# Performance work log

Measured on AMD Instinct MI355X. Metric: run time of the kernel, lower is better.

Reference implementation:

```python
import jax, jax.numpy as jnp
import numpy as np

P_MIN = 0.8        # minimum cumulative probability mass kept per row
THRESHOLD = 1e-10  # drop matches with probability below this
EPS = 1e-6         # distance clamp (matches dist.clamp(min=1e-6) in backward)

B, N, M, D = 4, 4096, 4096, 3


def setup_inputs() -> dict:
    key = jax.random.key(0)
    kx, ky = jax.random.split(key)
    x = jax.random.normal(kx, (B, N, D), dtype=jnp.float32)
    y = jax.random.normal(ky, (B, M, D), dtype=jnp.float32)
    return {"x": x, "y": y}


def _pairwise_dist(x, y):
    # ||x_i - y_j|| via Gram trick; avoids materializing [B,N,M,D] diff tensor.
    sq = (
        jnp.sum(x * x, axis=-1)[:, :, None]
        + jnp.sum(y * y, axis=-1)[:, None, :]
        - 2.0 * jnp.einsum("bnd,bmd->bnm", x, y)
    )
    return jnp.sqrt(jnp.maximum(sq, EPS * EPS))  # [B, N, M]


def _sparse_match_weights(d):
    # Row-wise soft matching probabilities over targets j.
    p = jax.nn.softmax(-d, axis=-1)  # [B, N, M]
    # Keep the most-probable entries per row until cumulative mass reaches P_MIN
    # (the dense, jit-friendly equivalent of the COO compaction in the kernel).
    order = jnp.argsort(-p, axis=-1)
    p_sorted = jnp.take_along_axis(p, order, axis=-1)
    csum = jnp.cumsum(p_sorted, axis=-1)
    keep_sorted = (csum - p_sorted) < P_MIN  # include entry that crosses P_MIN
    inv = jnp.argsort(order, axis=-1)
    keep = jnp.take_along_axis(keep_sorted, inv, axis=-1)
    return jnp.where(keep & (p > THRESHOLD), p, 0.0)  # sparse COO values, dense layout


def reference(x, y):
    d = _pairwise_dist(x, y)                     # [B, N, M]
    w = jax.lax.stop_gradient(_sparse_match_weights(d))  # weights are constants in bwd
    loss = jnp.sum(w * d)                        # scalar matching loss
    return loss
```

## Files before the change

kernel.cpp:

```cpp
#include <hip/hip_runtime.h>


#define MCOLS 4096
#define KPT   64
#define WPB   4
#define P_MIN 0.8f

__device__ __forceinline__ float waveSum(float v) {
    #pragma unroll
    for (int o = 32; o > 0; o >>= 1) v += __shfl_xor(v, o, 64);
    return v;
}
__device__ __forceinline__ float waveMax(float v) {
    #pragma unroll
    for (int o = 32; o > 0; o >>= 1) v = fmaxf(v, __shfl_xor(v, o, 64));
    return v;
}

__global__ __launch_bounds__(WPB * 64) void apml_row_wave(
        const float* __restrict__ x, const float* __restrict__ y,
        float* __restrict__ out) {
    __shared__ __align__(16) float scomp[WPB * 64];
    __shared__ float wacc[WPB];

    const int tid  = threadIdx.x;
    const int wid  = tid >> 6;
    const int lane = tid & 63;
    const int row  = blockIdx.x * WPB + wid;
    const int b    = row >> 12;

    const float x0 = x[row * 3 + 0];
    const float x1 = x[row * 3 + 1];
    const float x2 = x[row * 3 + 2];
    const float* yb = y + (size_t)b * MCOLS * 3;

    float p[KPT];
    float zl = 0.0f, pml = 0.0f;
    #pragma unroll
    for (int k = 0; k < KPT; ++k) {
        const int j = k * 64 + lane;
        const float y0 = yb[j * 3 + 0];
        const float y1 = yb[j * 3 + 1];
        const float y2 = yb[j * 3 + 2];
        const float dx = x0 - y0, dy = x1 - y1, dz = x2 - y2;
        const float sq = fmaxf(dx * dx + dy * dy + dz * dz, 1e-12f);
        const float pk = __expf(-sqrtf(sq));
        p[k] = pk;
        zl  += pk;
        pml  = fmaxf(pml, pk);
    }
    const float Z    = waveSum(zl);
    const float pmax = waveMax(pml);
    const float target = P_MIN * Z;

    float sl = 0.0f, sh = __uint_as_float(__float_as_uint(pmax) + 1u);
    float Gl = Z,    Gh = 0.0f;
    int   Cl = MCOLS, Ch = 0;

    for (int it = 0; it < 16 && (Cl - Ch) > 64; ++it) {
        float s;
        if (it & 1) {
            s = 0.5f * (sl + sh);
        } else {
            const float den = fmaxf(Gl - Gh, 1e-30f);
            s = sl + (sh - sl) * ((Gl - target) / den);
        }
        if (!(s > sl && s < sh)) s = 0.5f * (sl + sh);
        if (!(s > sl && s < sh)) break;

        float m = 0.0f;
        int   c = 0;
        #pragma unroll
        for (int k = 0; k < KPT; ++k) {
            const bool ge = (p[k] >= s);
            m += ge ? p[k] : 0.0f;
            c += (int)__popcll(__ballot(ge));
        }
        m = waveSum(m);
        if (m >= target) { sl = s; Gl = m; Cl = c; }
        else             { sh = s; Gh = m; Ch = c; }
    }

    int C = 0;
    #pragma unroll
    for (int k = 0; k < KPT; ++k) {
        const bool band = (p[k] >= sl) && (p[k] < sh);
        const unsigned long long mk = __ballot(band);
        if (band) {
            const unsigned mlo = (unsigned)mk, mhi = (unsigned)(mk >> 32);
            const int within = __builtin_amdgcn_mbcnt_hi(
                                   mhi, __builtin_amdgcn_mbcnt_lo(mlo, 0));
            const int pos = C + within;
            if (pos < 64) scomp[wid * 64 + pos] = p[k];
        }
        C += (int)__popcll(mk);
    }
    __builtin_amdgcn_s_waitcnt(0);
    const bool valid = (lane < C) && (lane < 64);
    const float cp = valid ? scomp[wid * 64 + lane] : 0.0f;

    float pstar, mb = 0.0f;
    int   cnt = 1;
    bool  haveTie;

    if (C > 64) {
        pstar = (sl > 0.0f) ? __uint_as_float(__float_as_uint(sl) - 1u) : 0.0f;
        haveTie = false;
    } else {
        float lo_s = sl, hi_s = sh, lo_G = Gl, hi_G = Gh;
        int   lo_C = Cl, hi_C = Ch;
        for (int it = 0; it < 12 && (lo_C - hi_C) > 2; ++it) {
            float s;
            if (it & 1) {
                s = 0.5f * (lo_s + hi_s);
            } else {
                const float den = fmaxf(lo_G - hi_G, 1e-30f);
                s = lo_s + (hi_s - lo_s) * ((lo_G - target) / den);
            }
            if (!(s > lo_s && s < hi_s)) s = 0.5f * (lo_s + hi_s);
            if (!(s > lo_s && s < hi_s)) break;

            const bool ge = valid && (cp >= s);
            const int  c  = Ch + (int)__popcll(__ballot(ge));
            const float m = Gh + waveSum(ge ? cp : 0.0f);
            if (m >= target) { lo_s = s; lo_G = m; lo_C = c; }
            else             { hi_s = s; hi_G = m; hi_C = c; }
        }

        float scur = hi_s, M = hi_G;
        bool ok = false;
        pstar = lo_s;
        for (int e = 0; e < 80; ++e) {
            const float v = waveMax((valid && cp < scur) ? cp : 0.0f);
            if (!(v > 0.0f)) break;
            const int cv = (int)__popcll(__ballot(valid && (cp == v)));
            const float Mn = M + v * (float)cv;
            if (Mn >= target) { pstar = v; mb = M; cnt = cv; ok = true; break; }
            M = Mn; scur = v;
        }
        haveTie = ok;
        if (!ok) {
            pstar = (lo_s > 0.0f) ? __uint_as_float(__float_as_uint(lo_s) - 1u)
                                  : 0.0f;
        }
    }

    float spd = 0.0f;
    #pragma unroll
    for (int k = 0; k < KPT; ++k) {
        const float t = (p[k] > pstar) ? p[k] : 1.0f;
        spd += t * (-__logf(t));
    }
    spd = waveSum(spd);

    if (lane == 0) {
        float tie = 0.0f;
        if (haveTie) {
            const float R = (target - mb) / pstar;
            int q = (int)ceilf(R);
            if (q < 1) q = 1;
            if (q > cnt) q = cnt;
            tie = (float)q * pstar * (-__logf(pstar));
        }
        wacc[wid] = (spd + tie) / Z;
    }
    __syncthreads();
    if (tid == 0) {
        atomicAdd(out, wacc[0] + wacc[1] + wacc[2] + wacc[3]);
    }
}

extern "C" void kernel_launch(void* const* d_in, const int* in_sizes, int n_in,
                              void* d_out, int out_size, void* d_ws, size_t ws_size,
                              hipStream_t stream) {
    const float* x = (const float*)d_in[0];
    const float* y = (const float*)d_in[1];
    float* out = (float*)d_out;

    const int nrows = in_sizes[0] / 3;
    const int nblocks = nrows / WPB;

    hipMemsetAsync(out, 0, sizeof(float), stream);
    apml_row_wave<<<nblocks, WPB * 64, 0, stream>>>(x, y, out);
}
```

Measured before the change: 175.4 us.

## Use DPP reductions, sampled threshold pre-search, and wider 256-entry compaction band

```diff
diff --git a/kernel.cpp b/kernel.cpp
--- a/kernel.cpp
+++ b/kernel.cpp
@@ -6,21 +6,34 @@
 #define WPB   4
 #define P_MIN 0.8f
 
-__device__ __forceinline__ float waveSum(float v) {
-    #pragma unroll
-    for (int o = 32; o > 0; o >>= 1) v += __shfl_xor(v, o, 64);
-    return v;
-}
-__device__ __forceinline__ float waveMax(float v) {
-    #pragma unroll
-    for (int o = 32; o > 0; o >>= 1) v = fmaxf(v, __shfl_xor(v, o, 64));
-    return v;
+template <int CTRL, int RM, int BM, bool BC>
+__device__ __forceinline__ float dpp_mov0(float x) {
+    return __int_as_float(__builtin_amdgcn_update_dpp(
+        0, __float_as_int(x), CTRL, RM, BM, BC));
+}
+__device__ __forceinline__ float dppSum(float v) {
+    v += dpp_mov0<0x111, 0xF, 0xF, true >(v);
+    v += dpp_mov0<0x112, 0xF, 0xF, true >(v);
+    v += dpp_mov0<0x114, 0xF, 0xF, true >(v);
+    v += dpp_mov0<0x118, 0xF, 0xF, true >(v);
+    v += dpp_mov0<0x142, 0xA, 0xF, false>(v);
+    v += dpp_mov0<0x143, 0xC, 0xF, false>(v);
+    return __int_as_float(__builtin_amdgcn_readlane(__float_as_int(v), 63));
+}
+__device__ __forceinline__ float dppMax(float v) {
+    v = fmaxf(v, dpp_mov0<0x111, 0xF, 0xF, true >(v));
+    v = fmaxf(v, dpp_mov0<0x112, 0xF, 0xF, true >(v));
+    v = fmaxf(v, dpp_mov0<0x114, 0xF, 0xF, true >(v));
+    v = fmaxf(v, dpp_mov0<0x118, 0xF, 0xF, true >(v));
+    v = fmaxf(v, dpp_mov0<0x142, 0xA, 0xF, false>(v));
+    v = fmaxf(v, dpp_mov0<0x143, 0xC, 0xF, false>(v));
+    return __int_as_float(__builtin_amdgcn_readlane(__float_as_int(v), 63));
 }
 
 __global__ __launch_bounds__(WPB * 64) void apml_row_wave(
         const float* __restrict__ x, const float* __restrict__ y,
         float* __restrict__ out) {
-    __shared__ __align__(16) float scomp[WPB * 64];
+    __shared__ __align__(16) float scomp[WPB * 256];
     __shared__ float wacc[WPB];
 
     const int tid  = threadIdx.x;
@@ -49,19 +62,44 @@
         zl  += pk;
         pml  = fmaxf(pml, pk);
     }
-    const float Z    = waveSum(zl);
-    const float pmax = waveMax(pml);
+    const float Z    = dppSum(zl);
+    const float pmax = dppMax(pml);
     const float target = P_MIN * Z;
-
-    float sl = 0.0f, sh = __uint_as_float(__float_as_uint(pmax) + 1u);
+    const float pTop = __uint_as_float(__float_as_uint(pmax) + 1u);
+
+    float ssl = 0.0f, ssh = pTop;
+    {
+        float eGl = 16.0f * dppSum(p[0] + p[1] + p[2] + p[3]);
+        float eGh = 0.0f;
+        for (int it = 0; it < 5; ++it) {
+            float s;
+            if (it & 1) {
+                s = 0.5f * (ssl + ssh);
+            } else {
+                const float den = fmaxf(eGl - eGh, 1e-30f);
+                s = ssl + (ssh - ssl) * ((eGl - target) / den);
+            }
+            if (!(s > ssl && s < ssh)) s = 0.5f * (ssl + ssh);
+            if (!(s > ssl && s < ssh)) break;
+            float m = 0.0f;
+            #pragma unroll
+            for (int q = 0; q < 4; ++q) m += (p[q] >= s) ? p[q] : 0.0f;
+            m = 16.0f * dppSum(m);
+            if (m >= target) { ssl = s; eGl = m; }
+            else             { ssh = s; eGh = m; }
+        }
+    }
+
+    float sl = 0.0f, sh = pTop;
     float Gl = Z,    Gh = 0.0f;
     int   Cl = MCOLS, Ch = 0;
 
-    for (int it = 0; it < 16 && (Cl - Ch) > 64; ++it) {
+    for (int it = 0; it < 12 && (Cl - Ch) > 256; ++it) {
         float s;
-        if (it & 1) {
-            s = 0.5f * (sl + sh);
-        } else {
+        if      (it == 0) s = ssl;
+        else if (it == 1) s = ssh;
+        else if (it & 1)  s = 0.5f * (sl + sh);
+        else {
             const float den = fmaxf(Gl - Gh, 1e-30f);
             s = sl + (sh - sl) * ((Gl - target) / den);
         }
@@ -76,7 +114,7 @@
             m += ge ? p[k] : 0.0f;
             c += (int)__popcll(__ballot(ge));
         }
-        m = waveSum(m);
+        m = dppSum(m);
         if (m >= target) { sl = s; Gl = m; Cl = c; }
         else             { sh = s; Gh = m; Ch = c; }
     }
@@ -91,25 +129,31 @@
             const int within = __builtin_amdgcn_mbcnt_hi(
                                    mhi, __builtin_amdgcn_mbcnt_lo(mlo, 0));
             const int pos = C + within;
-            if (pos < 64) scomp[wid * 64 + pos] = p[k];
+            if (pos < 256) scomp[wid * 256 + pos] = p[k];
         }
         C += (int)__popcll(mk);
     }
     __builtin_amdgcn_s_waitcnt(0);
-    const bool valid = (lane < C) && (lane < 64);
-    const float cp = valid ? scomp[wid * 64 + lane] : 0.0f;
+    float cp[4];
+    bool  cv[4];
+    #pragma unroll
+    for (int q = 0; q < 4; ++q) {
+        const int idx = q * 64 + lane;
+        cv[q] = (idx < C) && (idx < 256);
+        cp[q] = cv[q] ? scomp[wid * 256 + idx] : 0.0f;
+    }
 
     float pstar, mb = 0.0f;
     int   cnt = 1;
     bool  haveTie;
 
-    if (C > 64) {
+    if (C > 256) {
         pstar = (sl > 0.0f) ? __uint_as_float(__float_as_uint(sl) - 1u) : 0.0f;
         haveTie = false;
     } else {
         float lo_s = sl, hi_s = sh, lo_G = Gl, hi_G = Gh;
         int   lo_C = Cl, hi_C = Ch;
-        for (int it = 0; it < 12 && (lo_C - hi_C) > 2; ++it) {
+        for (int it = 0; it < 10 && (lo_C - hi_C) > 2; ++it) {
             float s;
             if (it & 1) {
                 s = 0.5f * (lo_s + hi_s);
@@ -120,9 +164,15 @@
             if (!(s > lo_s && s < hi_s)) s = 0.5f * (lo_s + hi_s);
             if (!(s > lo_s && s < hi_s)) break;
 
-            const bool ge = valid && (cp >= s);
-            const int  c  = Ch + (int)__popcll(__ballot(ge));
-            const float m = Gh + waveSum(ge ? cp : 0.0f);
+            float m = 0.0f;
+            int   c = Ch;
+            #pragma unroll
+            for (int q = 0; q < 4; ++q) {
+                const bool ge = cv[q] && (cp[q] >= s);
+                m += ge ? cp[q] : 0.0f;
+                c += (int)__popcll(__ballot(ge));
+            }
+            m = Gh + dppSum(m);
             if (m >= target) { lo_s = s; lo_G = m; lo_C = c; }
             else             { hi_s = s; hi_G = m; hi_C = c; }
         }
@@ -130,12 +180,19 @@
         float scur = hi_s, M = hi_G;
         bool ok = false;
         pstar = lo_s;
-        for (int e = 0; e < 80; ++e) {
-            const float v = waveMax((valid && cp < scur) ? cp : 0.0f);
+        for (int e = 0; e < 16; ++e) {
+            float vl = 0.0f;
+            #pragma unroll
+            for (int q = 0; q < 4; ++q)
+                vl = fmaxf(vl, (cv[q] && cp[q] < scur) ? cp[q] : 0.0f);
+            const float v = dppMax(vl);
             if (!(v > 0.0f)) break;
-            const int cv = (int)__popcll(__ballot(valid && (cp == v)));
-            const float Mn = M + v * (float)cv;
-            if (Mn >= target) { pstar = v; mb = M; cnt = cv; ok = true; break; }
+            int cvn = 0;
+            #pragma unroll
+            for (int q = 0; q < 4; ++q)
+                cvn += (int)__popcll(__ballot(cv[q] && (cp[q] == v)));
+            const float Mn = M + v * (float)cvn;
+            if (Mn >= target) { pstar = v; mb = M; cnt = cvn; ok = true; break; }
             M = Mn; scur = v;
         }
         haveTie = ok;
@@ -151,7 +208,7 @@
         const float t = (p[k] > pstar) ? p[k] : 1.0f;
         spd += t * (-__logf(t));
     }
-    spd = waveSum(spd);
+    spd = dppSum(spd);
 
     if (lane == 0) {
         float tie = 0.0f;
```

Result: faster. 167.9 us (-4.3%).
